# Performance work log

Hardware: AMD Instinct MI355X
Metric: run time of the kernel (lower is better)

The kernel has to match this reference:

```python
import jax, jax.numpy as jnp
import numpy as np

B, C, G = 8, 64, 65536
IN_DIM, OUT_DIM = 64, 64
SLOPE = 0.1


def setup_inputs() -> dict:
    key = jax.random.key(0)
    ks = jax.random.split(key, 5)
    features = jax.random.normal(ks[0], (B, C, G), dtype=jnp.float32)
    # Conv2d(in*2, out, 1, bias=False) weights, squeezed to [out, in*2]
    W0 = jax.random.normal(ks[1], (OUT_DIM, IN_DIM * 2), dtype=jnp.float32) * (1.0 / np.sqrt(IN_DIM * 2))
    W1 = jax.random.normal(ks[2], (OUT_DIM, OUT_DIM * 2), dtype=jnp.float32) * (1.0 / np.sqrt(OUT_DIM * 2))
    W2 = jax.random.normal(ks[3], (OUT_DIM, OUT_DIM * 2), dtype=jnp.float32) * (1.0 / np.sqrt(OUT_DIM * 2))
    W3 = jax.random.normal(ks[4], (OUT_DIM, OUT_DIM * 2), dtype=jnp.float32) * (1.0 / np.sqrt(OUT_DIM * 2))
    return {"features": features, "W0": W0, "W1": W1, "W2": W2, "W3": W3}


def _layer(x, W):
    # x: [B, C, G]; tile the first group's features and build (x, x - x0)
    x0 = x[:, :, :1]                               # [B, C, 1]
    h = jnp.concatenate([x, x - x0], axis=1)       # [B, 2C, G]
    # 1x1 conv == pointwise linear over channels
    y = jnp.einsum("oc,bcg->bog", W, h)            # [B, O, G]
    return jax.nn.leaky_relu(y, negative_slope=SLOPE)


def reference(features, W0, W1, W2, W3):
    x = features
    for W in (W0, W1, W2, W3):
        x = _layer(x, W)
    return jnp.max(x, axis=-1)                     # [B, O]
```

## Files before the change

### kernel.cpp

```cpp
#include <hip/hip_runtime.h>


#define G_TOT 65536

typedef _Float16 hf2 __attribute__((ext_vector_type(2)));
typedef _Float16 hf4 __attribute__((ext_vector_type(4)));
typedef _Float16 hf8 __attribute__((ext_vector_type(8)));
typedef float float4_ __attribute__((ext_vector_type(4)));

static __device__ __forceinline__ hf2 pkh(float x, float y) {
    return __builtin_bit_cast(hf2, __builtin_amdgcn_cvt_pkrtz(x, y));
}


__global__ __launch_bounds__(256) void ge_prep(
    const float* __restrict__ feat,
    const float* __restrict__ W0, const float* __restrict__ W1,
    const float* __restrict__ W2, const float* __restrict__ W3,
    float* __restrict__ ws)
{
    const int tid = threadIdx.x;
    const int blk = blockIdx.x;
    __shared__ float lw[64][129];
    __shared__ float x0[2][64];

    if (blk == 8) {
        unsigned* maxenc = (unsigned*)(ws + 18432);
        maxenc[tid] = 0u; maxenc[tid + 256] = 0u;
        _Float16* wf = (_Float16*)ws;
        for (int ci = tid; ci < 8192; ci += 256) {
            int f = ci >> 8, ln = (ci >> 2) & 63, h2 = ci & 3;
            int l = f >> 3, mt = (f >> 1) & 3, pr = f & 1;
            int o = (mt << 4) + (ln & 15);
            int c = (pr << 5) + ((h2 >> 1) << 4) + ((ln >> 4) << 2) + ((h2 & 1) << 1);
            const float* Wl = (l == 0) ? W0 : (l == 1) ? W1 : (l == 2) ? W2 : W3;
            float a0 = Wl[o * 128 + c]     + Wl[o * 128 + 64 + c];
            float a1 = Wl[o * 128 + c + 1] + Wl[o * 128 + 64 + c + 1];
            *(hf2*)&wf[ci << 1] = pkh(a0, a1);
        }
        return;
    }

    const int b = blk;
    if (tid < 64) x0[0][tid] = feat[(size_t)(b * 64 + tid) * G_TOT];
    float* nbias = ws + 16384;
    for (int l = 0; l < 4; ++l) {
        const float* Wl = (l == 0) ? W0 : (l == 1) ? W1 : (l == 2) ? W2 : W3;
        for (int i = tid; i < 64 * 128; i += 256) lw[i >> 7][i & 127] = Wl[i];
        __syncthreads();
        if (tid < 64) {
            const int o = tid;
            const float* src = x0[l & 1];
            float s1 = 0.f, s2 = 0.f;
            for (int c = 0; c < 64; ++c) {
                float xv = src[c];
                s1 += lw[o][c] * xv;
                s2 += lw[o][64 + c] * xv;
            }
            nbias[b * 256 + l * 64 + o] = -s2;
            x0[(l & 1) ^ 1][o] = fmaxf(s1, 0.1f * s1);
        }
        __syncthreads();
    }
}

__global__ __launch_bounds__(256, 2) void ge_main(
    const float* __restrict__ feat,
    const float* __restrict__ ws_wf,
    const float* __restrict__ nbias,
    unsigned* __restrict__ maxenc)
{
    __shared__ float lbias[256];
    __shared__ float blockmax[4][64];
    const int tid = threadIdx.x;
    const int b = blockIdx.x >> 6;
    const int w = tid >> 6, lane = tid & 63, q = lane >> 4, n = lane & 15;

    lbias[tid] = nbias[(b << 8) + tid];

    hf8 wfr[4][4][2];
    {
        const hf8* wp = (const hf8*)ws_wf;
#pragma unroll
        for (int l = 0; l < 4; ++l)
#pragma unroll
            for (int mt = 0; mt < 4; ++mt)
#pragma unroll
                for (int pr = 0; pr < 2; ++pr)
                    wfr[l][mt][pr] = wp[((((((l << 2) + mt) << 1) + pr)) << 6) + lane];
    }

    const int g0 = ((blockIdx.x & 63) << 10) + (w << 8);
    const float* Xrow = feat + (size_t)b * 64 * G_TOT + (size_t)(q << 2) * G_TOT;

    float rmax[4][4];
#pragma unroll
    for (int mt = 0; mt < 4; ++mt)
#pragma unroll
        for (int j = 0; j < 4; ++j) rmax[mt][j] = -__builtin_inff();

    float nxt[16];
    {
        int gcol = g0 + n;
#pragma unroll
        for (int kf = 0; kf < 4; ++kf)
#pragma unroll
            for (int r = 0; r < 4; ++r)
                nxt[kf * 4 + r] = Xrow[(size_t)((kf << 4) + r) * G_TOT + gcol];
    }
    __syncthreads();

#pragma unroll 1
    for (int nt = 0; nt < 16; ++nt) {
        hf4 bf[4];
#pragma unroll
        for (int kf = 0; kf < 4; ++kf) {
            union { hf2 h2[2]; hf4 h4; } u;
            u.h2[0] = pkh(nxt[kf * 4 + 0], nxt[kf * 4 + 1]);
            u.h2[1] = pkh(nxt[kf * 4 + 2], nxt[kf * 4 + 3]);
            bf[kf] = u.h4;
        }
        if (nt < 15) {
            int gcol = g0 + ((nt + 1) << 4) + n;
#pragma unroll
            for (int kf = 0; kf < 4; ++kf)
#pragma unroll
                for (int r = 0; r < 4; ++r)
                    nxt[kf * 4 + r] = Xrow[(size_t)((kf << 4) + r) * G_TOT + gcol];
        }

#pragma unroll
        for (int l = 0; l < 4; ++l) {
            float4_ acc[4];
#pragma unroll
            for (int mt = 0; mt < 4; ++mt) {
                if (l < 3) {
                    acc[mt] = *(const float4_*)&lbias[(l << 6) + (mt << 4) + (q << 2)];
                } else {
                    acc[mt] = float4_{0.f, 0.f, 0.f, 0.f};
                }
            }
#pragma unroll
            for (int mt = 0; mt < 4; ++mt) {
#pragma unroll
                for (int pr = 0; pr < 2; ++pr) {
                    union { hf8 h8; hf4 h4[2]; } ua;
                    ua.h8 = wfr[l][mt][pr];
                    acc[mt] = __builtin_amdgcn_mfma_f32_16x16x16f16(ua.h4[0], bf[(pr << 1) + 0], acc[mt], 0, 0, 0);
                    acc[mt] = __builtin_amdgcn_mfma_f32_16x16x16f16(ua.h4[1], bf[(pr << 1) + 1], acc[mt], 0, 0, 0);
                }
            }
            if (l < 3) {
#pragma unroll
                for (int mt = 0; mt < 4; ++mt) {
                    union { hf2 h2[2]; hf4 h4; } u;
                    u.h2[0] = pkh(acc[mt][0], acc[mt][1]);
                    u.h2[1] = pkh(acc[mt][2], acc[mt][3]);
                    hf4 h = u.h4;
                    h = __builtin_elementwise_max(h, h * hf4{(_Float16)0.1f, (_Float16)0.1f, (_Float16)0.1f, (_Float16)0.1f});
                    bf[mt] = h;
                }
            } else {
#pragma unroll
                for (int mt = 0; mt < 4; ++mt)
#pragma unroll
                    for (int j = 0; j < 4; ++j)
                        rmax[mt][j] = fmaxf(rmax[mt][j], acc[mt][j]);
            }
        }
    }

#pragma unroll
    for (int mt = 0; mt < 4; ++mt)
#pragma unroll
        for (int j = 0; j < 4; ++j) {
            float v = rmax[mt][j];
            v = fmaxf(v, __shfl_xor(v, 1, 64));
            v = fmaxf(v, __shfl_xor(v, 2, 64));
            v = fmaxf(v, __shfl_xor(v, 4, 64));
            v = fmaxf(v, __shfl_xor(v, 8, 64));
            rmax[mt][j] = v;
        }
    if (n == 0) {
#pragma unroll
        for (int mt = 0; mt < 4; ++mt)
#pragma unroll
            for (int j = 0; j < 4; ++j)
                blockmax[w][(mt << 4) + (q << 2) + j] = rmax[mt][j];
    }
    __syncthreads();
    if (tid < 64) {
        float v = fmaxf(fmaxf(blockmax[0][tid], blockmax[1][tid]),
                        fmaxf(blockmax[2][tid], blockmax[3][tid]));
        unsigned s = __float_as_uint(v);
        unsigned enc = (s & 0x80000000u) ? ~s : (s | 0x80000000u);
        atomicMax(&maxenc[b * 64 + tid], enc);
    }
}

__global__ void ge_final(const unsigned* __restrict__ maxenc,
                         const float* __restrict__ nbias,
                         float* __restrict__ out)
{
    int i = threadIdx.x;
    if (i < 512) {
        unsigned u = maxenc[i];
        unsigned s = (u & 0x80000000u) ? (u ^ 0x80000000u) : ~u;
        float v = __uint_as_float(s) + nbias[((i >> 6) << 8) + 192 + (i & 63)];
        out[i] = fmaxf(v, 0.1f * v);
    }
}

extern "C" void kernel_launch(void* const* d_in, const int* in_sizes, int n_in,
                              void* d_out, int out_size, void* d_ws, size_t ws_size,
                              hipStream_t stream) {
    const float* feat = (const float*)d_in[0];
    const float* W0 = (const float*)d_in[1];
    const float* W1 = (const float*)d_in[2];
    const float* W2 = (const float*)d_in[3];
    const float* W3 = (const float*)d_in[4];
    float* ws = (float*)d_ws;
    unsigned* maxenc = (unsigned*)(ws + 18432);

    ge_prep<<<9, 256, 0, stream>>>(feat, W0, W1, W2, W3, ws);
    ge_main<<<512, 256, 0, stream>>>(feat, ws, ws + 16384, maxenc);
    ge_final<<<1, 512, 0, stream>>>(maxenc, ws + 16384, (float*)d_out);
}
```

Measured before the change: 217.4 us.

## Fuse weight prep and bias computation into main kernel, double-buffer loads

Removes the separate prep kernel. Each main block now folds the weights into fp16 MFMA fragments and computes the per-batch x0 bias chain itself, redundantly, through shared memory. The atomicMax reduction is replaced by per-block partial maxima written to the workspace and reduced in the final kernel. Feature loads are now double-buffered two tiles ahead to hide more memory latency. In exchange, every block repeats the prep work and register pressure grows from the second prefetch buffer.

Measured after the change: 237.8 us. 1.09x slower.

```diff
diff --git a/kernel.cpp b/kernel.cpp
--- a/kernel.cpp
+++ b/kernel.cpp
@@ -12,136 +12,112 @@
     return __builtin_bit_cast(hf2, __builtin_amdgcn_cvt_pkrtz(x, y));
 }
 
-
-__global__ __launch_bounds__(256) void ge_prep(
+__global__ __launch_bounds__(256, 2) void ge_fused(
     const float* __restrict__ feat,
     const float* __restrict__ W0, const float* __restrict__ W1,
     const float* __restrict__ W2, const float* __restrict__ W3,
     float* __restrict__ ws)
 {
-    const int tid = threadIdx.x;
-    const int blk = blockIdx.x;
-    __shared__ float lw[64][129];
-    __shared__ float x0[2][64];
-
-    if (blk == 8) {
-        unsigned* maxenc = (unsigned*)(ws + 18432);
-        maxenc[tid] = 0u; maxenc[tid + 256] = 0u;
-        _Float16* wf = (_Float16*)ws;
-        for (int ci = tid; ci < 8192; ci += 256) {
-            int f = ci >> 8, ln = (ci >> 2) & 63, h2 = ci & 3;
-            int l = f >> 3, mt = (f >> 1) & 3, pr = f & 1;
-            int o = (mt << 4) + (ln & 15);
-            int c = (pr << 5) + ((h2 >> 1) << 4) + ((ln >> 4) << 2) + ((h2 & 1) << 1);
-            const float* Wl = (l == 0) ? W0 : (l == 1) ? W1 : (l == 2) ? W2 : W3;
-            float a0 = Wl[o * 128 + c]     + Wl[o * 128 + 64 + c];
-            float a1 = Wl[o * 128 + c + 1] + Wl[o * 128 + 64 + c + 1];
-            *(hf2*)&wf[ci << 1] = pkh(a0, a1);
-        }
-        return;
-    }
-
-    const int b = blk;
-    if (tid < 64) x0[0][tid] = feat[(size_t)(b * 64 + tid) * G_TOT];
-    float* nbias = ws + 16384;
-    for (int l = 0; l < 4; ++l) {
-        const float* Wl = (l == 0) ? W0 : (l == 1) ? W1 : (l == 2) ? W2 : W3;
-        for (int i = tid; i < 64 * 128; i += 256) lw[i >> 7][i & 127] = Wl[i];
-        __syncthreads();
-        if (tid < 64) {
-            const int o = tid;
-            const float* src = x0[l & 1];
-            float s1 = 0.f, s2 = 0.f;
-            for (int c = 0; c < 64; ++c) {
-                float xv = src[c];
-                s1 += lw[o][c] * xv;
-                s2 += lw[o][64 + c] * xv;
-            }
-            nbias[b * 256 + l * 64 + o] = -s2;
-            x0[(l & 1) ^ 1][o] = fmaxf(s1, 0.1f * s1);
-        }
-        __syncthreads();
-    }
-}
-
-__global__ __launch_bounds__(256, 2) void ge_main(
-    const float* __restrict__ feat,
-    const float* __restrict__ ws_wf,
-    const float* __restrict__ nbias,
-    unsigned* __restrict__ maxenc)
-{
-    __shared__ float lbias[256];
+    __shared__ __align__(16) float stg[64][132];
+    __shared__ float xch[2][64];
+    __shared__ float part1[64][4];
+    __shared__ float part2[64][4];
+    __shared__ __align__(16) float lbias[192];
+    __shared__ float nb3[64];
     __shared__ float blockmax[4][64];
+
     const int tid = threadIdx.x;
     const int b = blockIdx.x >> 6;
     const int w = tid >> 6, lane = tid & 63, q = lane >> 4, n = lane & 15;
-
-    lbias[tid] = nbias[(b << 8) + tid];
-
-    hf8 wfr[4][4][2];
-    {
-        const hf8* wp = (const hf8*)ws_wf;
-#pragma unroll
-        for (int l = 0; l < 4; ++l)
-#pragma unroll
-            for (int mt = 0; mt < 4; ++mt)
-#pragma unroll
-                for (int pr = 0; pr < 2; ++pr)
-                    wfr[l][mt][pr] = wp[((((((l << 2) + mt) << 1) + pr)) << 6) + lane];
-    }
-
     const int g0 = ((blockIdx.x & 63) << 10) + (w << 8);
     const float* Xrow = feat + (size_t)b * 64 * G_TOT + (size_t)(q << 2) * G_TOT;
 
+    float nxtA[16], nxtB[16];
+    {
+        int ga = g0 + n;
+#pragma unroll
+        for (int kf = 0; kf < 4; ++kf)
+#pragma unroll
+            for (int r = 0; r < 4; ++r) {
+                size_t off = (size_t)((kf << 4) + r) * G_TOT;
+                nxtA[kf * 4 + r] = Xrow[off + ga];
+                nxtB[kf * 4 + r] = Xrow[off + ga + 16];
+            }
+    }
+    if (tid < 64) xch[0][tid] = feat[(size_t)(b * 64 + tid) * G_TOT];
+
+    hf8 wfr[4][4][2];
+#pragma unroll
+    for (int l = 0; l < 4; ++l) {
+        const float* Wl = (l == 0) ? W0 : (l == 1) ? W1 : (l == 2) ? W2 : W3;
+#pragma unroll
+        for (int k = 0; k < 8; ++k) {
+            int i = tid + (k << 8);
+            *(float4_*)&stg[i >> 5][(i & 31) << 2] =
+                *(const float4_*)&Wl[(i >> 5) * 128 + ((i & 31) << 2)];
+        }
+        __syncthreads();
+#pragma unroll
+        for (int mt = 0; mt < 4; ++mt)
+#pragma unroll
+            for (int pr = 0; pr < 2; ++pr) {
+                int o = (mt << 4) + n, base = (pr << 5) + (q << 2);
+                float4_ a0 = *(const float4_*)&stg[o][base];
+                float4_ a1 = *(const float4_*)&stg[o][base + 16];
+                float4_ c0 = *(const float4_*)&stg[o][base + 64];
+                float4_ c1 = *(const float4_*)&stg[o][base + 80];
+                a0 += c0; a1 += c1;
+                union { hf2 h2[4]; hf8 h8; } u;
+                u.h2[0] = pkh(a0[0], a0[1]); u.h2[1] = pkh(a0[2], a0[3]);
+                u.h2[2] = pkh(a1[0], a1[1]); u.h2[3] = pkh(a1[2], a1[3]);
+                wfr[l][mt][pr] = u.h8;
+            }
+        {
+            int o = tid & 63, cq = tid >> 6;
+            float s1 = 0.f, s2 = 0.f;
+            const float* xs = xch[l & 1];
+#pragma unroll
+            for (int c16 = 0; c16 < 16; ++c16) {
+                int c = (cq << 4) + c16;
+                float xv = xs[c];
+                s1 += stg[o][c] * xv;
+                s2 += stg[o][64 + c] * xv;
+            }
+            part1[o][cq] = s1; part2[o][cq] = s2;
+        }
+        __syncthreads();
+        if (tid < 64) {
+            float S1 = part1[tid][0] + part1[tid][1] + part1[tid][2] + part1[tid][3];
+            float S2 = part2[tid][0] + part2[tid][1] + part2[tid][2] + part2[tid][3];
+            if (l < 3) {
+                lbias[(l << 6) + tid] = -S2;
+                xch[(l & 1) ^ 1][tid] = fmaxf(S1, 0.1f * S1);
+            } else {
+                nb3[tid] = -S2;
+            }
+        }
+    }
+    __syncthreads();
+
     float rmax[4][4];
 #pragma unroll
     for (int mt = 0; mt < 4; ++mt)
 #pragma unroll
         for (int j = 0; j < 4; ++j) rmax[mt][j] = -__builtin_inff();
 
-    float nxt[16];
-    {
-        int gcol = g0 + n;
-#pragma unroll
-        for (int kf = 0; kf < 4; ++kf)
-#pragma unroll
-            for (int r = 0; r < 4; ++r)
-                nxt[kf * 4 + r] = Xrow[(size_t)((kf << 4) + r) * G_TOT + gcol];
-    }
-    __syncthreads();
-
-#pragma unroll 1
-    for (int nt = 0; nt < 16; ++nt) {
-        hf4 bf[4];
-#pragma unroll
-        for (int kf = 0; kf < 4; ++kf) {
-            union { hf2 h2[2]; hf4 h4; } u;
-            u.h2[0] = pkh(nxt[kf * 4 + 0], nxt[kf * 4 + 1]);
-            u.h2[1] = pkh(nxt[kf * 4 + 2], nxt[kf * 4 + 3]);
-            bf[kf] = u.h4;
-        }
-        if (nt < 15) {
-            int gcol = g0 + ((nt + 1) << 4) + n;
-#pragma unroll
-            for (int kf = 0; kf < 4; ++kf)
-#pragma unroll
-                for (int r = 0; r < 4; ++r)
-                    nxt[kf * 4 + r] = Xrow[(size_t)((kf << 4) + r) * G_TOT + gcol];
-        }
-
+    const hf4 k01 = { (_Float16)0.1f, (_Float16)0.1f, (_Float16)0.1f, (_Float16)0.1f };
+
+    auto compute = [&](hf4* bf) {
 #pragma unroll
         for (int l = 0; l < 4; ++l) {
             float4_ acc[4];
 #pragma unroll
             for (int mt = 0; mt < 4; ++mt) {
-                if (l < 3) {
-                    acc[mt] = *(const float4_*)&lbias[(l << 6) + (mt << 4) + (q << 2)];
-                } else {
-                    acc[mt] = float4_{0.f, 0.f, 0.f, 0.f};
-                }
-            }
-#pragma unroll
-            for (int mt = 0; mt < 4; ++mt) {
+                if (l < 3) acc[mt] = *(const float4_*)&lbias[(l << 6) + (mt << 4) + (q << 2)];
+                else       acc[mt] = float4_{0.f, 0.f, 0.f, 0.f};
+            }
+#pragma unroll
+            for (int mt = 0; mt < 4; ++mt)
 #pragma unroll
                 for (int pr = 0; pr < 2; ++pr) {
                     union { hf8 h8; hf4 h4[2]; } ua;
@@ -149,7 +125,6 @@
                     acc[mt] = __builtin_amdgcn_mfma_f32_16x16x16f16(ua.h4[0], bf[(pr << 1) + 0], acc[mt], 0, 0, 0);
                     acc[mt] = __builtin_amdgcn_mfma_f32_16x16x16f16(ua.h4[1], bf[(pr << 1) + 1], acc[mt], 0, 0, 0);
                 }
-            }
             if (l < 3) {
 #pragma unroll
                 for (int mt = 0; mt < 4; ++mt) {
@@ -157,7 +132,7 @@
                     u.h2[0] = pkh(acc[mt][0], acc[mt][1]);
                     u.h2[1] = pkh(acc[mt][2], acc[mt][3]);
                     hf4 h = u.h4;
-                    h = __builtin_elementwise_max(h, h * hf4{(_Float16)0.1f, (_Float16)0.1f, (_Float16)0.1f, (_Float16)0.1f});
+                    h = __builtin_elementwise_max(h, h * k01);
                     bf[mt] = h;
                 }
             } else {
@@ -168,6 +143,44 @@
                         rmax[mt][j] = fmaxf(rmax[mt][j], acc[mt][j]);
             }
         }
+    };
+
+#pragma unroll 1
+    for (int nt = 0; nt < 16; nt += 2) {
+        hf4 bf[4];
+#pragma unroll
+        for (int kf = 0; kf < 4; ++kf) {
+            union { hf2 h2[2]; hf4 h4; } u;
+            u.h2[0] = pkh(nxtA[kf * 4 + 0], nxtA[kf * 4 + 1]);
+            u.h2[1] = pkh(nxtA[kf * 4 + 2], nxtA[kf * 4 + 3]);
+            bf[kf] = u.h4;
+        }
+        if (nt < 14) {
+            int gcol = g0 + ((nt + 2) << 4) + n;
+#pragma unroll
+            for (int kf = 0; kf < 4; ++kf)
+#pragma unroll
+                for (int r = 0; r < 4; ++r)
+                    nxtA[kf * 4 + r] = Xrow[(size_t)((kf << 4) + r) * G_TOT + gcol];
+        }
+        compute(bf);
+
+#pragma unroll
+        for (int kf = 0; kf < 4; ++kf) {
+            union { hf2 h2[2]; hf4 h4; } u;
+            u.h2[0] = pkh(nxtB[kf * 4 + 0], nxtB[kf * 4 + 1]);
+            u.h2[1] = pkh(nxtB[kf * 4 + 2], nxtB[kf * 4 + 3]);
+            bf[kf] = u.h4;
+        }
+        if (nt < 14) {
+            int gcol = g0 + ((nt + 3) << 4) + n;
+#pragma unroll
+            for (int kf = 0; kf < 4; ++kf)
+#pragma unroll
+                for (int r = 0; r < 4; ++r)
+                    nxtB[kf * 4 + r] = Xrow[(size_t)((kf << 4) + r) * G_TOT + gcol];
+        }
+        compute(bf);
     }
 
 #pragma unroll
@@ -192,21 +205,22 @@
     if (tid < 64) {
         float v = fmaxf(fmaxf(blockmax[0][tid], blockmax[1][tid]),
                         fmaxf(blockmax[2][tid], blockmax[3][tid]));
-        unsigned s = __float_as_uint(v);
-        unsigned enc = (s & 0x80000000u) ? ~s : (s | 0x80000000u);
-        atomicMax(&maxenc[b * 64 + tid], enc);
-    }
-}
-
-__global__ void ge_final(const unsigned* __restrict__ maxenc,
-                         const float* __restrict__ nbias,
-                         float* __restrict__ out)
+        ws[(size_t)blockIdx.x * 64 + tid] = v;
+        if ((blockIdx.x & 63) == 0) ws[32768 + (b << 6) + tid] = nb3[tid];
+    }
+}
+
+__global__ void ge_final(const float* __restrict__ ws, float* __restrict__ out)
 {
     int i = threadIdx.x;
     if (i < 512) {
-        unsigned u = maxenc[i];
-        unsigned s = (u & 0x80000000u) ? (u ^ 0x80000000u) : ~u;
-        float v = __uint_as_float(s) + nbias[((i >> 6) << 8) + 192 + (i & 63)];
+        int b = i >> 6, o = i & 63;
+        const float* base = ws + (size_t)(b << 6) * 64 + o;
+        float m = -__builtin_inff();
+#pragma unroll
+        for (int blk = 0; blk < 64; ++blk)
+            m = fmaxf(m, base[blk * 64]);
+        float v = m + ws[32768 + i];
         out[i] = fmaxf(v, 0.1f * v);
     }
 }
@@ -220,9 +234,7 @@
     const float* W2 = (const float*)d_in[3];
     const float* W3 = (const float*)d_in[4];
     float* ws = (float*)d_ws;
-    unsigned* maxenc = (unsigned*)(ws + 18432);
-
-    ge_prep<<<9, 256, 0, stream>>>(feat, W0, W1, W2, W3, ws);
-    ge_main<<<512, 256, 0, stream>>>(feat, ws, ws + 16384, maxenc);
-    ge_final<<<1, 512, 0, stream>>>(maxenc, ws + 16384, (float*)d_out);
-}
+
+    ge_fused<<<512, 256, 0, stream>>>(feat, W0, W1, W2, W3, ws);
+    ge_final<<<1, 512, 0, stream>>>(ws, (float*)d_out);
+}
```

## Load float2 per lane and process two column tiles per iteration

Applied to the files above, without the earlier changes.

Each lane now loads two adjacent G columns as float2 instead of one float, so a 16-lane group covers 32 contiguous columns. The loop runs 8 groups of two interleaved 16-column tiles instead of 16 single tiles. This halves the number of load instructions, widens each memory access, and gives more independent MFMA work per prefetch. The first loads are also issued before the weight fragment loads and the bias barrier. Column-to-lane assignment changes, which is harmless because only a max over columns is taken, but the doubled buffer and second accumulator chain may add register pressure.

Measured after the change: 222.4 us. +2.3%, slower.

```diff
diff --git a/kernel.cpp b/kernel.cpp
--- a/kernel.cpp
+++ b/kernel.cpp
@@ -6,6 +6,7 @@
 typedef _Float16 hf2 __attribute__((ext_vector_type(2)));
 typedef _Float16 hf4 __attribute__((ext_vector_type(4)));
 typedef _Float16 hf8 __attribute__((ext_vector_type(8)));
+typedef float float2_ __attribute__((ext_vector_type(2)));
 typedef float float4_ __attribute__((ext_vector_type(4)));
 
 static __device__ __forceinline__ hf2 pkh(float x, float y) {
@@ -64,6 +65,44 @@
     }
 }
 
+#define COMPUTE_TILE(BF)                                                              \
+    _Pragma("unroll")                                                                 \
+    for (int l = 0; l < 4; ++l) {                                                     \
+        float4_ acc[4];                                                               \
+        _Pragma("unroll")                                                             \
+        for (int mt = 0; mt < 4; ++mt) {                                              \
+            if (l < 3) acc[mt] = *(const float4_*)&lbias[(l << 6) + (mt << 4) + (q << 2)]; \
+            else       acc[mt] = float4_{0.f, 0.f, 0.f, 0.f};                         \
+        }                                                                             \
+        _Pragma("unroll")                                                             \
+        for (int mt = 0; mt < 4; ++mt) {                                              \
+            _Pragma("unroll")                                                         \
+            for (int pr = 0; pr < 2; ++pr) {                                          \
+                union { hf8 h8; hf4 h4[2]; } ua;                                      \
+                ua.h8 = wfr[l][mt][pr];                                               \
+                acc[mt] = __builtin_amdgcn_mfma_f32_16x16x16f16(ua.h4[0], BF[(pr << 1) + 0], acc[mt], 0, 0, 0); \
+                acc[mt] = __builtin_amdgcn_mfma_f32_16x16x16f16(ua.h4[1], BF[(pr << 1) + 1], acc[mt], 0, 0, 0); \
+            }                                                                         \
+        }                                                                             \
+        if (l < 3) {                                                                  \
+            _Pragma("unroll")                                                         \
+            for (int mt = 0; mt < 4; ++mt) {                                          \
+                union { hf2 h2[2]; hf4 h4; } u;                                       \
+                u.h2[0] = pkh(acc[mt][0], acc[mt][1]);                                \
+                u.h2[1] = pkh(acc[mt][2], acc[mt][3]);                                \
+                hf4 h = u.h4;                                                         \
+                h = __builtin_elementwise_max(h, h * k01);                            \
+                BF[mt] = h;                                                           \
+            }                                                                         \
+        } else {                                                                      \
+            _Pragma("unroll")                                                         \
+            for (int mt = 0; mt < 4; ++mt)                                            \
+                _Pragma("unroll")                                                     \
+                for (int j = 0; j < 4; ++j)                                           \
+                    rmax[mt][j] = fmaxf(rmax[mt][j], acc[mt][j]);                     \
+        }                                                                             \
+    }
+
 __global__ __launch_bounds__(256, 2) void ge_main(
     const float* __restrict__ feat,
     const float* __restrict__ ws_wf,
@@ -75,8 +114,17 @@
     const int tid = threadIdx.x;
     const int b = blockIdx.x >> 6;
     const int w = tid >> 6, lane = tid & 63, q = lane >> 4, n = lane & 15;
-
-    lbias[tid] = nbias[(b << 8) + tid];
+    const int g0 = ((blockIdx.x & 63) << 10) + (w << 8);
+
+    const float* Xbase = feat + (size_t)b * 64 * G_TOT + (size_t)(q << 2) * G_TOT
+                       + (size_t)g0 + (size_t)(n << 1);
+
+    float2_ buf[16];
+#pragma unroll
+    for (int kf = 0; kf < 4; ++kf)
+#pragma unroll
+        for (int r = 0; r < 4; ++r)
+            buf[kf * 4 + r] = *(const float2_*)&Xbase[(size_t)((kf << 4) + r) * G_TOT];
 
     hf8 wfr[4][4][2];
     {
@@ -90,8 +138,8 @@
                     wfr[l][mt][pr] = wp[((((((l << 2) + mt) << 1) + pr)) << 6) + lane];
     }
 
-    const int g0 = ((blockIdx.x & 63) << 10) + (w << 8);
-    const float* Xrow = feat + (size_t)b * 64 * G_TOT + (size_t)(q << 2) * G_TOT;
+    lbias[tid] = nbias[(b << 8) + tid];
+    __syncthreads();
 
     float rmax[4][4];
 #pragma unroll
@@ -99,75 +147,31 @@
 #pragma unroll
         for (int j = 0; j < 4; ++j) rmax[mt][j] = -__builtin_inff();
 
-    float nxt[16];
-    {
-        int gcol = g0 + n;
-#pragma unroll
-        for (int kf = 0; kf < 4; ++kf)
-#pragma unroll
-            for (int r = 0; r < 4; ++r)
-                nxt[kf * 4 + r] = Xrow[(size_t)((kf << 4) + r) * G_TOT + gcol];
-    }
-    __syncthreads();
+    const hf4 k01 = { (_Float16)0.1f, (_Float16)0.1f, (_Float16)0.1f, (_Float16)0.1f };
 
 #pragma unroll 1
-    for (int nt = 0; nt < 16; ++nt) {
-        hf4 bf[4];
+    for (int grp = 0; grp < 8; ++grp) {
+        hf4 bfA[4], bfB[4];
 #pragma unroll
         for (int kf = 0; kf < 4; ++kf) {
-            union { hf2 h2[2]; hf4 h4; } u;
-            u.h2[0] = pkh(nxt[kf * 4 + 0], nxt[kf * 4 + 1]);
-            u.h2[1] = pkh(nxt[kf * 4 + 2], nxt[kf * 4 + 3]);
-            bf[kf] = u.h4;
-        }
-        if (nt < 15) {
-            int gcol = g0 + ((nt + 1) << 4) + n;
+            union { hf2 h2[2]; hf4 h4; } ua, ub;
+            ua.h2[0] = pkh(buf[kf * 4 + 0][0], buf[kf * 4 + 1][0]);
+            ua.h2[1] = pkh(buf[kf * 4 + 2][0], buf[kf * 4 + 3][0]);
+            ub.h2[0] = pkh(buf[kf * 4 + 0][1], buf[kf * 4 + 1][1]);
+            ub.h2[1] = pkh(buf[kf * 4 + 2][1], buf[kf * 4 + 3][1]);
+            bfA[kf] = ua.h4;
+            bfB[kf] = ub.h4;
+        }
+        if (grp < 7) {
+            const float* Xp = Xbase + ((grp + 1) << 5);
 #pragma unroll
             for (int kf = 0; kf < 4; ++kf)
 #pragma unroll
                 for (int r = 0; r < 4; ++r)
-                    nxt[kf * 4 + r] = Xrow[(size_t)((kf << 4) + r) * G_TOT + gcol];
-        }
-
-#pragma unroll
-        for (int l = 0; l < 4; ++l) {
-            float4_ acc[4];
-#pragma unroll
-            for (int mt = 0; mt < 4; ++mt) {
-                if (l < 3) {
-                    acc[mt] = *(const float4_*)&lbias[(l << 6) + (mt << 4) + (q << 2)];
-                } else {
-                    acc[mt] = float4_{0.f, 0.f, 0.f, 0.f};
-                }
-            }
-#pragma unroll
-            for (int mt = 0; mt < 4; ++mt) {
-#pragma unroll
-                for (int pr = 0; pr < 2; ++pr) {
-                    union { hf8 h8; hf4 h4[2]; } ua;
-                    ua.h8 = wfr[l][mt][pr];
-                    acc[mt] = __builtin_amdgcn_mfma_f32_16x16x16f16(ua.h4[0], bf[(pr << 1) + 0], acc[mt], 0, 0, 0);
-                    acc[mt] = __builtin_amdgcn_mfma_f32_16x16x16f16(ua.h4[1], bf[(pr << 1) + 1], acc[mt], 0, 0, 0);
-                }
-            }
-            if (l < 3) {
-#pragma unroll
-                for (int mt = 0; mt < 4; ++mt) {
-                    union { hf2 h2[2]; hf4 h4; } u;
-                    u.h2[0] = pkh(acc[mt][0], acc[mt][1]);
-                    u.h2[1] = pkh(acc[mt][2], acc[mt][3]);
-                    hf4 h = u.h4;
-                    h = __builtin_elementwise_max(h, h * hf4{(_Float16)0.1f, (_Float16)0.1f, (_Float16)0.1f, (_Float16)0.1f});
-                    bf[mt] = h;
-                }
-            } else {
-#pragma unroll
-                for (int mt = 0; mt < 4; ++mt)
-#pragma unroll
-                    for (int j = 0; j < 4; ++j)
-                        rmax[mt][j] = fmaxf(rmax[mt][j], acc[mt][j]);
-            }
-        }
+                    buf[kf * 4 + r] = *(const float2_*)&Xp[(size_t)((kf << 4) + r) * G_TOT];
+        }
+        COMPUTE_TILE(bfA)
+        COMPUTE_TILE(bfB)
     }
 
 #pragma unroll
```

## Fuse final max decode into main kernel via last-block counter

Applied to the files above, without the earlier changes.

Removes the separate ge_final launch. The last block of ge_main to finish, detected through an atomic counter, now decodes the max values and writes the output. The prep kernel loads all four weight matrices into shared memory up front with float4 reads instead of reloading per layer, and the main kernel remaps block indices so batches are interleaved across blocks. This saves one kernel launch and some prep latency, at the cost of extra fences and atomics at the end of each block and a much larger shared-memory footprint in prep.

Measured after the change: 231.5 us. +6.5%, slower.

```diff
diff --git a/kernel.cpp b/kernel.cpp
--- a/kernel.cpp
+++ b/kernel.cpp
@@ -11,7 +11,6 @@
 static __device__ __forceinline__ hf2 pkh(float x, float y) {
     return __builtin_bit_cast(hf2, __builtin_amdgcn_cvt_pkrtz(x, y));
 }
-
 
 __global__ __launch_bounds__(256) void ge_prep(
     const float* __restrict__ feat,
@@ -21,12 +20,11 @@
 {
     const int tid = threadIdx.x;
     const int blk = blockIdx.x;
-    __shared__ float lw[64][129];
-    __shared__ float x0[2][64];
 
     if (blk == 8) {
         unsigned* maxenc = (unsigned*)(ws + 18432);
         maxenc[tid] = 0u; maxenc[tid + 256] = 0u;
+        if (tid == 0) *(unsigned*)(ws + 18944) = 0u;
         _Float16* wf = (_Float16*)ws;
         for (int ci = tid; ci < 8192; ci += 256) {
             int f = ci >> 8, ln = (ci >> 2) & 63, h2 = ci & 3;
@@ -41,21 +39,33 @@
         return;
     }
 
+    __shared__ float lw4[4][64][129];
+    __shared__ float x0[2][64];
     const int b = blk;
     if (tid < 64) x0[0][tid] = feat[(size_t)(b * 64 + tid) * G_TOT];
+#pragma unroll
+    for (int l = 0; l < 4; ++l) {
+        const float* Wl = (l == 0) ? W0 : (l == 1) ? W1 : (l == 2) ? W2 : W3;
+#pragma unroll
+        for (int k = 0; k < 8; ++k) {
+            int i = tid + (k << 8);
+            int o = i >> 5, c = (i & 31) << 2;
+            float4_ v = *(const float4_*)&Wl[o * 128 + c];
+            lw4[l][o][c] = v[0]; lw4[l][o][c + 1] = v[1];
+            lw4[l][o][c + 2] = v[2]; lw4[l][o][c + 3] = v[3];
+        }
+    }
+    __syncthreads();
     float* nbias = ws + 16384;
     for (int l = 0; l < 4; ++l) {
-        const float* Wl = (l == 0) ? W0 : (l == 1) ? W1 : (l == 2) ? W2 : W3;
-        for (int i = tid; i < 64 * 128; i += 256) lw[i >> 7][i & 127] = Wl[i];
-        __syncthreads();
         if (tid < 64) {
             const int o = tid;
             const float* src = x0[l & 1];
             float s1 = 0.f, s2 = 0.f;
             for (int c = 0; c < 64; ++c) {
                 float xv = src[c];
-                s1 += lw[o][c] * xv;
-                s2 += lw[o][64 + c] * xv;
+                s1 += lw4[l][o][c] * xv;
+                s2 += lw4[l][o][64 + c] * xv;
             }
             nbias[b * 256 + l * 64 + o] = -s2;
             x0[(l & 1) ^ 1][o] = fmaxf(s1, 0.1f * s1);
@@ -68,12 +78,17 @@
     const float* __restrict__ feat,
     const float* __restrict__ ws_wf,
     const float* __restrict__ nbias,
-    unsigned* __restrict__ maxenc)
+    unsigned* __restrict__ maxenc,
+    unsigned* __restrict__ counter,
+    float* __restrict__ out)
 {
     __shared__ float lbias[256];
     __shared__ float blockmax[4][64];
+    __shared__ unsigned lastflag;
     const int tid = threadIdx.x;
-    const int b = blockIdx.x >> 6;
+
+    const int nb = ((blockIdx.x & 7) << 6) | (blockIdx.x >> 3);
+    const int b = nb >> 6;
     const int w = tid >> 6, lane = tid & 63, q = lane >> 4, n = lane & 15;
 
     lbias[tid] = nbias[(b << 8) + tid];
@@ -90,7 +105,7 @@
                     wfr[l][mt][pr] = wp[((((((l << 2) + mt) << 1) + pr)) << 6) + lane];
     }
 
-    const int g0 = ((blockIdx.x & 63) << 10) + (w << 8);
+    const int g0 = ((nb & 63) << 10) + (w << 8);
     const float* Xrow = feat + (size_t)b * 64 * G_TOT + (size_t)(q << 2) * G_TOT;
 
     float rmax[4][4];
@@ -134,11 +149,8 @@
             float4_ acc[4];
 #pragma unroll
             for (int mt = 0; mt < 4; ++mt) {
-                if (l < 3) {
-                    acc[mt] = *(const float4_*)&lbias[(l << 6) + (mt << 4) + (q << 2)];
-                } else {
-                    acc[mt] = float4_{0.f, 0.f, 0.f, 0.f};
-                }
+                if (l < 3) acc[mt] = *(const float4_*)&lbias[(l << 6) + (mt << 4) + (q << 2)];
+                else       acc[mt] = float4_{0.f, 0.f, 0.f, 0.f};
             }
 #pragma unroll
             for (int mt = 0; mt < 4; ++mt) {
@@ -196,18 +208,24 @@
         unsigned enc = (s & 0x80000000u) ? ~s : (s | 0x80000000u);
         atomicMax(&maxenc[b * 64 + tid], enc);
     }
-}
-
-__global__ void ge_final(const unsigned* __restrict__ maxenc,
-                         const float* __restrict__ nbias,
-                         float* __restrict__ out)
-{
-    int i = threadIdx.x;
-    if (i < 512) {
-        unsigned u = maxenc[i];
-        unsigned s = (u & 0x80000000u) ? (u ^ 0x80000000u) : ~u;
-        float v = __uint_as_float(s) + nbias[((i >> 6) << 8) + 192 + (i & 63)];
-        out[i] = fmaxf(v, 0.1f * v);
+
+    __syncthreads();
+    if (tid == 0) {
+        __threadfence();
+        unsigned c = atomicAdd(counter, 1u);
+        lastflag = (c == 511u);
+    }
+    __syncthreads();
+    if (lastflag) {
+        __threadfence();
+#pragma unroll
+        for (int k = 0; k < 2; ++k) {
+            int i = tid + (k << 8);
+            unsigned u = atomicOr(&maxenc[i], 0u);
+            unsigned s = (u & 0x80000000u) ? (u ^ 0x80000000u) : ~u;
+            float v = __uint_as_float(s) + nbias[((i >> 6) << 8) + 192 + (i & 63)];
+            out[i] = fmaxf(v, 0.1f * v);
+        }
     }
 }
 
@@ -221,8 +239,8 @@
     const float* W3 = (const float*)d_in[4];
     float* ws = (float*)d_ws;
     unsigned* maxenc = (unsigned*)(ws + 18432);
+    unsigned* counter = (unsigned*)(ws + 18944);
 
     ge_prep<<<9, 256, 0, stream>>>(feat, W0, W1, W2, W3, ws);
-    ge_main<<<512, 256, 0, stream>>>(feat, ws, ws + 16384, maxenc);
-    ge_final<<<1, 512, 0, stream>>>(maxenc, ws + 16384, (float*)d_out);
-}
+    ge_main<<<512, 256, 0, stream>>>(feat, ws, ws + 16384, maxenc, counter, (float*)d_out);
+}
```
